# Kernel optimization log

Measured on AMD Instinct MI355X. Metric: run time of the kernel, lower is better.

## Reference

```python
import jax, jax.numpy as jnp
import numpy as np

CLIP = 50.0

def _lstm_layer(xs, w_ih, w_hh, b, h0, c0):
    # xs: [B, T, D]; precompute input projection for all timesteps (same math)
    x_proj = jnp.einsum('btd,gd->btg', xs, w_ih) + b  # [B, T, 4H]
    x_proj_t = jnp.transpose(x_proj, (1, 0, 2))        # [T, B, 4H]
    H = h0.shape[-1]

    def step(carry, xg):
        h, c = carry
        gates = xg + h @ w_hh.T                        # [B, 4H]
        i, f, o, g = jnp.split(gates, 4, axis=1)
        i = jax.nn.sigmoid(i); f = jax.nn.sigmoid(f)
        o = jax.nn.sigmoid(o); g = jnp.tanh(g)
        new_c = f * c + i * g
        new_h = o * jnp.tanh(new_c)
        # clip states (matches clip_states, applied after h uses unclipped c)
        new_c = jnp.clip(new_c, -CLIP, CLIP)
        new_h = jnp.clip(new_h, -CLIP, CLIP)
        return (new_h, new_c), new_h

    (hT, cT), ys = jax.lax.scan(step, (h0, c0), x_proj_t)
    return jnp.transpose(ys, (1, 0, 2)), hT, cT        # [B, T, H]


def setup_inputs() -> dict:
    key = jax.random.key(0)
    ks = jax.random.split(key, 6)
    B, T, D, H = 64, 1024, 256, 512
    u = lambda k, shape: jax.random.uniform(k, shape, jnp.float32, -0.1, 0.1)
    return {
        'x': jax.random.normal(ks[0], (B, T, D), jnp.float32),
        'w_ih0': u(ks[1], (4 * H, D)),
        'w_hh0': u(ks[2], (4 * H, H)),
        'b0': jnp.zeros((4 * H,), jnp.float32),
        'w_ih1': u(ks[3], (4 * H, H)),
        'w_hh1': u(ks[4], (4 * H, H)),
        'b1': jnp.zeros((4 * H,), jnp.float32),
    }


def reference(x, w_ih0, w_hh0, b0, w_ih1, w_hh1, b1):
    B = x.shape[0]
    H = w_hh0.shape[1]
    h0 = jnp.zeros((B, H), x.dtype)
    c0 = jnp.zeros((B, H), x.dtype)
    y0, h_l0, c_l0 = _lstm_layer(x, w_ih0, w_hh0, b0, h0, c0)
    y1, h_l1, c_l1 = _lstm_layer(y0, w_ih1, w_hh1, b1, h0, c0)
    h = jnp.stack([h_l0, h_l1], axis=0)  # [L, B, H]
    c = jnp.stack([c_l0, c_l1], axis=0)
    return y1, (h, c)
```

## Files before the change

kernel.cpp:

```cpp
#include <hip/hip_runtime.h>

#define BDIM 64
#define TDIM 1024
#define DDIM 256
#define HDIM 512
#define RING 4

typedef unsigned short ushort_t;
typedef unsigned int uint32;
typedef unsigned long long ull;
typedef __attribute__((ext_vector_type(8))) short short8;
typedef __attribute__((ext_vector_type(4))) float f32x4;
typedef __attribute__((ext_vector_type(4))) uint32 u32x4;

__device__ __forceinline__ ushort_t f2bf(float f) {
  union { float f; uint32 u; } v; v.f = f;
  uint32 u = v.u;
  return (ushort_t)((u + 0x7fffu + ((u >> 16) & 1u)) >> 16);
}

__device__ __forceinline__ short8 pack8(float4 a, float4 b) {
  short8 s;
  s[0] = (short)f2bf(a.x); s[1] = (short)f2bf(a.y);
  s[2] = (short)f2bf(a.z); s[3] = (short)f2bf(a.w);
  s[4] = (short)f2bf(b.x); s[5] = (short)f2bf(b.y);
  s[6] = (short)f2bf(b.z); s[7] = (short)f2bf(b.w);
  return s;
}

__device__ __forceinline__ ull pack4bf(f32x4 v) {
  return (ull)f2bf(v[0]) | ((ull)f2bf(v[1]) << 16)
       | ((ull)f2bf(v[2]) << 32) | ((ull)f2bf(v[3]) << 48);
}

__device__ __forceinline__ float sigm(float x) { return 1.0f / (1.0f + __expf(-x)); }
__device__ __forceinline__ float tanh_fast(float x) { return 1.0f - 2.0f / (__expf(2.0f * x) + 1.0f); }

__device__ __forceinline__ uint32 ld_sc1(uint32* p) {
  return __hip_atomic_load(p, __ATOMIC_RELAXED, __HIP_MEMORY_SCOPE_AGENT);
}
__device__ __forceinline__ void st_sc1(uint32* p, uint32 v) {
  __hip_atomic_store(p, v, __ATOMIC_RELAXED, __HIP_MEMORY_SCOPE_AGENT);
}

__device__ __forceinline__ void wave_poll_sc1(uint32* fl, uint32 tgt) {
  int it = 0;
  for (;;) {
    uint32 v = ld_sc1(fl);
    if (__all((int)(v >= tgt))) break;
    __builtin_amdgcn_s_sleep(1);
    if (++it > 60000) break;
  }
  asm volatile("" ::: "memory");
}

__device__ __forceinline__ int frag_off(int row, int kf, int lg) {
  return kf * 512 + (((lg * 16 + row) ^ (kf & 7)) << 3);
}

__device__ __forceinline__ void ds_stage(ushort_t* dst, int tid, const ull* v) {
  const int s = tid & 15, h = (tid >> 4) & 3, wvq = tid >> 6;
#pragma unroll
  for (int q = 0; q < 8; ++q) {
    const int row = wvq * 4 + (q & 3);
    const int kf  = ((q >> 2) << 3) | ((s >> 1) & 7);
    *(ull*)&dst[frag_off(row, kf, h) + (s & 1) * 4] = v[q];
  }
}

__device__ __forceinline__ size_t chunk_off(int tid) {
  const int s = tid & 15, h = (tid >> 4) & 3, wvq = tid >> 6;
  return (size_t)(wvq * 4) * 2048
       + (size_t)(((((s >> 1) & 7) * 8) + h * 2 + (s & 1)) * 16);
}

__device__ __forceinline__ void load_tagged_8(const char* buf, int tid, uint32 expect, ull* v) {
  const char* base  = buf + chunk_off(tid);
  const char* base2 = base + 4096;
  u32x4 c0, c1, c2, c3, c4v, c5, c6, c7;
  int it = 0;
  for (;;) {
    asm volatile(
        "global_load_dwordx4 %0, %8, off sc0 sc1\n\t"
        "global_load_dwordx4 %1, %8, off offset:1024 sc0 sc1\n\t"
        "global_load_dwordx4 %2, %8, off offset:2048 sc0 sc1\n\t"
        "global_load_dwordx4 %3, %8, off offset:3072 sc0 sc1\n\t"
        "global_load_dwordx4 %4, %9, off sc0 sc1\n\t"
        "global_load_dwordx4 %5, %9, off offset:1024 sc0 sc1\n\t"
        "global_load_dwordx4 %6, %9, off offset:2048 sc0 sc1\n\t"
        "global_load_dwordx4 %7, %9, off offset:3072 sc0 sc1\n\t"
        "s_waitcnt vmcnt(0)"
        : "=&v"(c0), "=&v"(c1), "=&v"(c2), "=&v"(c3),
          "=&v"(c4v), "=&v"(c5), "=&v"(c6), "=&v"(c7)
        : "v"(base), "v"(base2) : "memory");
    bool ok = (c0.z == expect) & (c1.z == expect) & (c2.z == expect) & (c3.z == expect)
            & (c4v.z == expect) & (c5.z == expect) & (c6.z == expect) & (c7.z == expect);
    if (ok) break;
    if (++it > 30000) break;
  }
  v[0] = ((ull)c0.y << 32) | c0.x;   v[4] = ((ull)c1.y << 32) | c1.x;
  v[1] = ((ull)c2.y << 32) | c2.x;   v[5] = ((ull)c3.y << 32) | c3.x;
  v[2] = ((ull)c4v.y << 32) | c4v.x; v[6] = ((ull)c5.y << 32) | c5.x;
  v[3] = ((ull)c6.y << 32) | c6.x;   v[7] = ((ull)c7.y << 32) | c7.x;
}

#define BT_BYTES   32768
#define SLOT_BYTES (4 * BT_BYTES)

__global__ void __launch_bounds__(256, 1)
lstm_fused(const float* __restrict__ x,
           const float* __restrict__ w_ih0, const float* __restrict__ w_hh0,
           const float* __restrict__ b0,
           const float* __restrict__ w_ih1, const float* __restrict__ w_hh1,
           const float* __restrict__ b1,
           float* __restrict__ out,
           uint32* consF, char* ringT, char* h1T)
{
  const int b     = (int)blockIdx.x;
  const int g     = b & 7;
  const int layer = g >> 2;
  const int bt    = g & 3;
  const int ct    = b >> 3;
  const int tid   = (int)threadIdx.x;
  const int wv    = tid >> 6;
  const int lane  = tid & 63;
  const int lr    = lane & 15;
  const int lg    = lane >> 4;

  __shared__ __align__(16) ushort_t Is[16 * 512];
  __shared__ __align__(16) ushort_t Hs[16 * 512];
  __shared__ __align__(16) float gates[4][16][16];

  const int NI  = layer ? 16 : 8;
  const int Din = layer ? HDIM : DDIM;
  const float* wih = layer ? w_ih1 : w_ih0;
  const float* whh = layer ? w_hh1 : w_hh0;
  const float* bb  = layer ? b1 : b0;
  const int grow = wv * HDIM + ct * 16 + lr;

  short8 wf[32];
#pragma unroll
  for (int kf = 0; kf < 32; ++kf) wf[kf] = (short8)((short)0);
#pragma unroll
  for (int kf = 0; kf < 32; ++kf) {
    if (kf < NI + 16) {
      const float* src;
      if (kf < NI) src = wih + (size_t)grow * Din + (size_t)kf * 32 + lg * 8;
      else         src = whh + (size_t)grow * HDIM + (size_t)(kf - NI) * 32 + lg * 8;
      float4 a = *(const float4*)(src);
      float4 bq = *(const float4*)(src + 4);
      wf[kf] = pack8(a, bq);
    }
  }
  const float bias = bb[grow];

  float c4[4] = {0.f, 0.f, 0.f, 0.f};
  float4 xp0, xp1, xp2, xp3;
  ull rv[8];
  const int xr = tid >> 4;
  const int xcb = tid & 15;

  if (layer == 0) {
    const float4* xv = (const float4*)(x + (size_t)(bt * 16 + xr) * (TDIM * DDIM) + xcb * 16);
    xp0 = xv[0]; xp1 = xv[1]; xp2 = xv[2]; xp3 = xv[3];
  } else {
    load_tagged_8(ringT + (size_t)bt * BT_BYTES, tid, 1u, rv);
  }

  for (int t = 0; t < TDIM; ++t) {
    if (layer == 0 && wv == 1 && t >= RING)
      wave_poll_sc1(consF + bt * 32 + (lane & 31), (uint32)(t - RING + 1));

    if (layer == 0) {
      {
        const int c0 = xcb * 16;
        *(short8*)&Is[frag_off(xr, c0 >> 5, (c0 >> 3) & 3)] = pack8(xp0, xp1);
        const int c1 = c0 + 8;
        *(short8*)&Is[frag_off(xr, c1 >> 5, (c1 >> 3) & 3)] = pack8(xp2, xp3);
      }
      if (t > 0) {
        ull hv[8];
        load_tagged_8(ringT + (size_t)((t - 1) & (RING - 1)) * SLOT_BYTES
                      + (size_t)bt * BT_BYTES, tid, (uint32)t, hv);
        ds_stage(Hs, tid, hv);
      }
    } else {
      ds_stage(Is, tid, rv);
      if (t > 0) {
        ull hv[8];
        load_tagged_8(h1T + (size_t)((t - 1) & 1) * SLOT_BYTES
                      + (size_t)bt * BT_BYTES, tid, (uint32)t, hv);
        ds_stage(Hs, tid, hv);
      }
    }
    __syncthreads();
    if (layer == 1 && tid == 0)
      st_sc1(consF + bt * 32 + ct, (uint32)(t + 1));

    f32x4 acc0 = {0.f, 0.f, 0.f, 0.f}, acc1 = {0.f, 0.f, 0.f, 0.f};
#pragma unroll
    for (int kf = 0; kf < 16; ++kf) {
      if (kf < NI) {
        const short8 af = *(const short8*)&Is[frag_off(lr, kf, lg)];
        if (kf & 1) acc1 = __builtin_amdgcn_mfma_f32_16x16x32_bf16(af, wf[kf], acc1, 0, 0, 0);
        else        acc0 = __builtin_amdgcn_mfma_f32_16x16x32_bf16(af, wf[kf], acc0, 0, 0, 0);
      }
    }
    if (t > 0) {
#pragma unroll
      for (int kf = 0; kf < 16; ++kf) {
        const short8 af = *(const short8*)&Hs[frag_off(lr, kf, lg)];
        if (kf & 1) acc1 = __builtin_amdgcn_mfma_f32_16x16x32_bf16(af, wf[NI + kf], acc1, 0, 0, 0);
        else        acc0 = __builtin_amdgcn_mfma_f32_16x16x32_bf16(af, wf[NI + kf], acc0, 0, 0, 0);
      }
    }
#pragma unroll
    for (int i = 0; i < 4; ++i) {
      float v = acc0[i] + acc1[i] + bias;
      float a = (wv < 3) ? sigm(v) : tanh_fast(v);
      gates[wv][lg * 4 + i][lr] = a;
    }
    __syncthreads();

    if (layer == 0 && wv != 0 && t + 1 < TDIM) {
      const float4* xv = (const float4*)(x + (size_t)(bt * 16 + xr) * (TDIM * DDIM)
                                           + (size_t)(t + 1) * DDIM + xcb * 16);
      xp0 = xv[0]; xp1 = xv[1]; xp2 = xv[2]; xp3 = xv[3];
    }
    if (layer == 1 && wv != 0 && t + 1 < TDIM) {
      load_tagged_8(ringT + (size_t)((t + 1) & (RING - 1)) * SLOT_BYTES
                    + (size_t)bt * BT_BYTES, tid, (uint32)(t + 2), rv);
    }
    if (wv == 0) {
      const int r  = lane >> 2;
      const int cg = lane & 3;
      f32x4 gi = *(const f32x4*)&gates[0][r][cg * 4];
      f32x4 gf = *(const f32x4*)&gates[1][r][cg * 4];
      f32x4 go = *(const f32x4*)&gates[2][r][cg * 4];
      f32x4 gg = *(const f32x4*)&gates[3][r][cg * 4];
      f32x4 nh4, nc4;
#pragma unroll
      for (int k = 0; k < 4; ++k) {
        float nc = gf[k] * c4[k] + gi[k] * gg[k];
        float nh = go[k] * tanh_fast(nc);
        nc = fminf(fmaxf(nc, -50.f), 50.f);
        nh = fminf(fmaxf(nh, -50.f), 50.f);
        c4[k] = nc; nh4[k] = nh; nc4[k] = nc;
      }
      const ull hv = pack4bf(nh4);
      u32x4 pub;
      pub.x = (uint32)hv; pub.y = (uint32)(hv >> 32);
      pub.z = (uint32)(t + 1); pub.w = 0u;
      char* dst = (layer == 0)
          ? ringT + (size_t)(t & (RING - 1)) * SLOT_BYTES + (size_t)bt * BT_BYTES
          : h1T + (size_t)(t & 1) * SLOT_BYTES + (size_t)bt * BT_BYTES;
      dst += (size_t)r * 2048 + (size_t)(ct * 4 + cg) * 16;
      asm volatile("global_store_dwordx4 %0, %1, off sc0 sc1"
                   :: "v"(dst), "v"(pub) : "memory");
      if (layer == 1)
        *(f32x4*)&out[(size_t)(bt * 16 + r) * (TDIM * HDIM) + (size_t)t * HDIM + ct * 16 + cg * 4] = nh4;
      if (t == TDIM - 1) {
        const size_t OH = (size_t)BDIM * TDIM * HDIM;
        const size_t OC = OH + 2 * (size_t)BDIM * HDIM;
        *(f32x4*)&out[OH + (size_t)layer * BDIM * HDIM + (size_t)(bt * 16 + r) * HDIM + ct * 16 + cg * 4] = nh4;
        *(f32x4*)&out[OC + (size_t)layer * BDIM * HDIM + (size_t)(bt * 16 + r) * HDIM + ct * 16 + cg * 4] = nc4;
      }
      if (layer == 0 && t + 1 < TDIM) {
        const float4* xv = (const float4*)(x + (size_t)(bt * 16 + xr) * (TDIM * DDIM)
                                             + (size_t)(t + 1) * DDIM + xcb * 16);
        xp0 = xv[0]; xp1 = xv[1]; xp2 = xv[2]; xp3 = xv[3];
      }
      if (layer == 1 && t + 1 < TDIM) {
        load_tagged_8(ringT + (size_t)((t + 1) & (RING - 1)) * SLOT_BYTES
                      + (size_t)bt * BT_BYTES, tid, (uint32)(t + 2), rv);
      }
    }
  }
}

extern "C" void kernel_launch(void* const* d_in, const int* in_sizes, int n_in,
                              void* d_out, int out_size, void* d_ws, size_t ws_size,
                              hipStream_t stream) {
  (void)in_sizes; (void)n_in; (void)out_size; (void)ws_size;
  const float* x     = (const float*)d_in[0];
  const float* w_ih0 = (const float*)d_in[1];
  const float* w_hh0 = (const float*)d_in[2];
  const float* b0    = (const float*)d_in[3];
  const float* w_ih1 = (const float*)d_in[4];
  const float* w_hh1 = (const float*)d_in[5];
  const float* b1    = (const float*)d_in[6];
  float* out = (float*)d_out;

  char* ws = (char*)d_ws;
  uint32* consF = (uint32*)(ws + 0);
  char* ringT = ws + 8192;
  char* h1T   = ws + 8192 + 4 * SLOT_BYTES;

  hipMemsetAsync(ws, 0, 8192, stream);
  hipMemsetAsync(ws + 8192, 0, 6 * SLOT_BYTES, stream);
  lstm_fused<<<dim3(256), dim3(256), 0, stream>>>(
      x, w_ih0, w_hh0, b0, w_ih1, w_hh1, b1, out, consF, ringT, h1T);
}
```

Before: 2.513 ms.

## Prefetch layer-1 input ring slot into LDS via async global_load_lds

After: 2.943 ms. 1.17x slower.

```diff
diff --git a/kernel.cpp b/kernel.cpp
--- a/kernel.cpp
+++ b/kernel.cpp
@@ -130,6 +130,7 @@
   __shared__ __align__(16) ushort_t Is[16 * 512];
   __shared__ __align__(16) ushort_t Hs[16 * 512];
   __shared__ __align__(16) float gates[4][16][16];
+  __shared__ __align__(16) ull raw[2048 * 2];
 
   const int NI  = layer ? 16 : 8;
   const int Din = layer ? HDIM : DDIM;
@@ -156,15 +157,13 @@
 
   float c4[4] = {0.f, 0.f, 0.f, 0.f};
   float4 xp0, xp1, xp2, xp3;
-  ull rv[8];
   const int xr = tid >> 4;
   const int xcb = tid & 15;
+  const int s_ = tid & 15, h_ = (tid >> 4) & 3;
 
   if (layer == 0) {
     const float4* xv = (const float4*)(x + (size_t)(bt * 16 + xr) * (TDIM * DDIM) + xcb * 16);
     xp0 = xv[0]; xp1 = xv[1]; xp2 = xv[2]; xp3 = xv[3];
-  } else {
-    load_tagged_8(ringT + (size_t)bt * BT_BYTES, tid, 1u, rv);
   }
 
   for (int t = 0; t < TDIM; ++t) {
@@ -185,7 +184,43 @@
         ds_stage(Hs, tid, hv);
       }
     } else {
-      ds_stage(Is, tid, rv);
+      if (t == 0) {
+        ull rv[8];
+        load_tagged_8(ringT + (size_t)bt * BT_BYTES, tid, 1u, rv);
+        ds_stage(Is, tid, rv);
+      } else {
+        asm volatile("s_waitcnt vmcnt(0)" ::: "memory");
+        ull hv8[8];
+        int okm = 1;
+        const uint32 expect = (uint32)(t + 1);
+        const int c_lo = (((s_ >> 1) & 7) * 8) + h_ * 2 + (s_ & 1);
+#pragma unroll
+        for (int q = 0; q < 8; ++q) {
+          const int row = wv * 4 + (q & 3);
+          const int G = row * 128 + ((q >> 2) << 6) + c_lo;
+          const int i = G ^ ((G >> 3) & 7);
+          u32x4 cc = *(const u32x4*)&raw[(size_t)i * 2];
+          hv8[q] = ((ull)cc.y << 32) | cc.x;
+          okm &= (int)(cc.z == expect);
+        }
+        if (!okm)
+          load_tagged_8(ringT + (size_t)(t & (RING - 1)) * SLOT_BYTES
+                        + (size_t)bt * BT_BYTES, tid, expect, hv8);
+        ds_stage(Is, tid, hv8);
+      }
+      if (t + 1 < TDIM) {
+        const char* slot = ringT + (size_t)((t + 1) & (RING - 1)) * SLOT_BYTES
+                         + (size_t)bt * BT_BYTES;
+#pragma unroll
+        for (int j = 0; j < 8; ++j) {
+          const int i = wv * 512 + j * 64 + lane;
+          const int G = i ^ ((i >> 3) & 7);
+          __builtin_amdgcn_global_load_lds(
+              (const __attribute__((address_space(1))) uint32*)(slot + (size_t)G * 16),
+              (__attribute__((address_space(3))) uint32*)&raw[(size_t)(wv * 512 + j * 64) * 2],
+              16, 0, 17 );
+        }
+      }
       if (t > 0) {
         ull hv[8];
         load_tagged_8(h1T + (size_t)((t - 1) & 1) * SLOT_BYTES
@@ -226,10 +261,6 @@
       const float4* xv = (const float4*)(x + (size_t)(bt * 16 + xr) * (TDIM * DDIM)
                                            + (size_t)(t + 1) * DDIM + xcb * 16);
       xp0 = xv[0]; xp1 = xv[1]; xp2 = xv[2]; xp3 = xv[3];
-    }
-    if (layer == 1 && wv != 0 && t + 1 < TDIM) {
-      load_tagged_8(ringT + (size_t)((t + 1) & (RING - 1)) * SLOT_BYTES
-                    + (size_t)bt * BT_BYTES, tid, (uint32)(t + 2), rv);
     }
     if (wv == 0) {
       const int r  = lane >> 2;
@@ -270,10 +301,6 @@
                                              + (size_t)(t + 1) * DDIM + xcb * 16);
         xp0 = xv[0]; xp1 = xv[1]; xp2 = xv[2]; xp3 = xv[3];
       }
-      if (layer == 1 && t + 1 < TDIM) {
-        load_tagged_8(ringT + (size_t)((t + 1) & (RING - 1)) * SLOT_BYTES
-                      + (size_t)bt * BT_BYTES, tid, (uint32)(t + 2), rv);
-      }
     }
   }
 }
```
